# Kernel tuning notes

Hardware: AMD Instinct MI355X
Metric: run time of the kernel (lower is better)

## Reference

```python
import jax, jax.numpy as jnp
import numpy as np

B, S, HID = 2, 2048, 4096
NH, D = 32, 128          # heads, head_dim
G, GS = 8, 4             # palu groups, group_size (heads per group)
RK = 256                 # rank per K group (rank_k[i])
RV = 2048                # total V rank
FGD = RV // G            # fused_group_dim = 256
FH = FGD * NH            # fused_hidden_dim = 8192
GD = HID // G            # k group_dim = 512
THETA = 10000.0


def setup_inputs() -> dict:
    key = jax.random.key(0)
    ks = jax.random.split(key, 7)
    hidden_states = jax.random.normal(ks[0], (B, S, HID), jnp.float32)
    causal = jnp.tril(jnp.ones((S, S), bool))
    attention_mask = jnp.broadcast_to(
        jnp.where(causal, 0.0, -1e9).astype(jnp.float32)[None, None], (B, 1, S, S))
    position_ids = jnp.broadcast_to(jnp.arange(S, dtype=jnp.int32)[None], (B, S))
    sc = 0.02
    Wq = sc * jax.random.normal(ks[1], (HID, HID), jnp.float32)
    WVT = sc * jax.random.normal(ks[2], (G * RK, HID), jnp.float32)   # k_proj.VT
    U = sc * jax.random.normal(ks[3], (GD, G * RK), jnp.float32)      # k_proj.U
    Wv = sc * jax.random.normal(ks[4], (RV, HID), jnp.float32)
    Wo = sc * jax.random.normal(ks[5], (HID, FH), jnp.float32)
    return dict(hidden_states=hidden_states, attention_mask=attention_mask,
                position_ids=position_ids, Wq=Wq, WVT=WVT, U=U, Wv=Wv, Wo=Wo)


def _rotate_half(x):
    return jnp.concatenate([-x[..., D // 2:], x[..., :D // 2]], axis=-1)


def reference(hidden_states, attention_mask, position_ids, Wq, WVT, U, Wv, Wo):
    b, q, _ = hidden_states.shape
    # projections
    qs = (hidden_states @ Wq.T).reshape(b, q, NH, D).transpose(0, 2, 1, 3)      # (b,H,q,d)
    k_lat = (hidden_states @ WVT.T).reshape(b, q, G, RK).transpose(0, 2, 1, 3)  # (b,G,q,RK)
    v_lat = (hidden_states @ Wv.T).reshape(b, q, G, FGD).transpose(0, 2, 1, 3)  # (b,G,q,FGD)
    # headwise reconstruction of K: group g latent (RK) -> group_dim (512) via U[:, g-slice]
    Ug = U.reshape(GD, G, RK)
    keys = jnp.einsum('bgsr,dgr->bgsd', k_lat, Ug)                 # (b,G,q,512)
    keys = keys.transpose(0, 2, 1, 3).reshape(b, q, NH, D).transpose(0, 2, 1, 3)  # (b,H,q,d)
    # RoPE
    inv_freq = 1.0 / (THETA ** (jnp.arange(0, D, 2, dtype=jnp.float32) / D))
    freqs = position_ids.astype(jnp.float32)[..., None] * inv_freq            # (b,q,d/2)
    emb = jnp.concatenate([freqs, freqs], axis=-1)
    cos, sin = jnp.cos(emb)[:, None], jnp.sin(emb)[:, None]                   # (b,1,q,d)
    qs = qs * cos + _rotate_half(qs) * sin
    keys = keys * cos + _rotate_half(keys) * sin
    # attention scores + mask + fp32 softmax
    attn = jnp.einsum('bhqd,bhkd->bhqk', qs, keys) / np.sqrt(D).astype(np.float32)
    attn = attn + attention_mask
    attn = jax.nn.softmax(attn.astype(jnp.float32), axis=-1).astype(qs.dtype)
    # PALU fused low-rank V path: exact torch reshape/transpose semantics
    aw = attn.reshape(b, G, q * GS, q)                                        # (b,G,gs*q,kv)
    out = jnp.einsum('bgik,bgkf->bgif', aw, v_lat)                            # (b,G,gs*q,FGD)
    out = out.transpose(0, 2, 1, 3).reshape(b, q, FH)                         # (b,q,8192)
    return out @ Wo.T
```

## Files before the change

### kernel.cpp

```cpp
#include <hip/hip_runtime.h>
#include <hip/hip_bf16.h>

typedef __hip_bfloat16 bf16;
typedef __bf16 bf16x8 __attribute__((ext_vector_type(8)));
typedef float f32x4 __attribute__((ext_vector_type(4)));

#define MFMA16(a, b, c) __builtin_amdgcn_mfma_f32_16x16x32_bf16(a, b, c, 0, 0, 0)

__device__ __forceinline__ void llds16(const bf16* g, bf16* lds) {
  __builtin_amdgcn_global_load_lds(
      (const __attribute__((address_space(1))) unsigned int*)g,
      (__attribute__((address_space(3))) unsigned int*)lds, 16, 0, 0);
}

__device__ __forceinline__ void storeC(float* p, float v) { *p = v; }
__device__ __forceinline__ void storeC(bf16* p, float v) { *p = __float2bfloat16(v); }

__global__ __launch_bounds__(256) void cvt_f2b(const float* __restrict__ in,
                                               bf16* __restrict__ out, int n4) {
  int i = blockIdx.x * 256 + threadIdx.x;
  if (i >= n4) return;
  float4 v = ((const float4*)in)[i];
  union { bf16 h[4]; short4 s; } u;
  u.h[0] = __float2bfloat16(v.x);
  u.h[1] = __float2bfloat16(v.y);
  u.h[2] = __float2bfloat16(v.z);
  u.h[3] = __float2bfloat16(v.w);
  ((short4*)out)[i] = u.s;
}

template <typename OUT_T>
__global__ __launch_bounds__(512, 2) void gemm256(
    const bf16* __restrict__ A, const bf16* __restrict__ B, OUT_T* __restrict__ C,
    int K, int lda, int ldb, int ldc) {
  extern __shared__ bf16 sm[];
  const int t = threadIdx.x, w = t >> 6, l = t & 63;
  const int lane_r = l & 15, quad = l >> 4;
  const int wm = (w >> 2) * 128, wn = (w & 3) * 64;
  const long m0 = (long)blockIdx.y * 256, n0 = (long)blockIdx.x * 256;
  const int r0 = t >> 2;
  const int c0 = (((t & 3) ^ (r0 & 3)) << 3);
  const bf16* As0 = A + (m0 + r0) * lda + c0;
  const bf16* As1 = A + (m0 + r0 + 128) * lda + c0;
  const bf16* Bs0 = B + (n0 + r0) * ldb + c0;
  const bf16* Bs1 = B + (n0 + r0 + 128) * ldb + c0;

#define STAGE(sl, kt)                                   \
  do {                                                  \
    long ko = (long)(kt) * 32;                          \
    bf16* dA = sm + (sl) * 16384;                       \
    bf16* dB = dA + 8192;                               \
    llds16(As0 + ko, dA + t * 8);                       \
    llds16(As1 + ko, dA + (t + 512) * 8);               \
    llds16(Bs0 + ko, dB + t * 8);                       \
    llds16(Bs1 + ko, dB + (t + 512) * 8);               \
  } while (0)

  f32x4 acc[8][4] = {};
  const int KT = K >> 5;
  const int sw = quad ^ (lane_r & 3);

  STAGE(0, 0);
  STAGE(1, 1);
  int sl = 0;
  for (int kt = 0; kt < KT; ++kt) {
    const int pre = KT - 1 - kt;
    if (pre >= 2) {
      int sl2 = sl + 2;
      if (sl2 >= 3) sl2 -= 3;
      STAGE(sl2, kt + 2);
      asm volatile("s_waitcnt vmcnt(8)" ::: "memory");
    } else if (pre == 1) {
      asm volatile("s_waitcnt vmcnt(4)" ::: "memory");
    } else {
      asm volatile("s_waitcnt vmcnt(0)" ::: "memory");
    }
    __builtin_amdgcn_s_barrier();
    __builtin_amdgcn_sched_barrier(0);
    const bf16* Al = sm + sl * 16384;
    const bf16* Bl = Al + 8192;
    bf16x8 af[8], bfr[4];
#pragma unroll
    for (int mt = 0; mt < 8; ++mt)
      af[mt] = *(const bf16x8*)&Al[(wm + mt * 16 + lane_r) * 32 + sw * 8];
#pragma unroll
    for (int nt = 0; nt < 4; ++nt)
      bfr[nt] = *(const bf16x8*)&Bl[(wn + nt * 16 + lane_r) * 32 + sw * 8];
    __builtin_amdgcn_s_setprio(1);
#pragma unroll
    for (int mt = 0; mt < 8; ++mt)
#pragma unroll
      for (int nt = 0; nt < 4; ++nt)
        acc[mt][nt] = MFMA16(af[mt], bfr[nt], acc[mt][nt]);
    __builtin_amdgcn_s_setprio(0);
    __builtin_amdgcn_s_barrier();
    if (++sl == 3) sl = 0;
  }
#undef STAGE

#pragma unroll
  for (int mt = 0; mt < 8; ++mt)
#pragma unroll
    for (int nt = 0; nt < 4; ++nt) {
      long row = m0 + wm + mt * 16 + quad * 4;
      long col = n0 + wn + nt * 16 + lane_r;
#pragma unroll
      for (int r = 0; r < 4; ++r) storeC(&C[(row + r) * ldc + col], acc[mt][nt][r]);
    }
}

template <typename OUT_T>
__global__ __launch_bounds__(256) void gemm_bt(
    const bf16* __restrict__ A, const bf16* __restrict__ B, OUT_T* __restrict__ C,
    int M, int N, int K, int lda, int ldb, int ldc,
    long batchA, long batchB, long batchC) {
  __shared__ alignas(16) bf16 As[128 * 32];
  __shared__ alignas(16) bf16 Bs[128 * 32];
  const int t = threadIdx.x;
  const int w = t >> 6, l = t & 63;
  const int lane_r = l & 15, quad = l >> 4;
  const int wm = (w >> 1) * 64, wn = (w & 1) * 64;
  const long m0 = (long)blockIdx.y * 128, n0 = (long)blockIdx.x * 128;
  A += (long)blockIdx.z * batchA;
  B += (long)blockIdx.z * batchB;
  C += (long)blockIdx.z * batchC;
  const int r0a = t >> 2;
  const int cba = (t & 3) * 8;
  f32x4 acc[4][4] = {};
  for (int k0 = 0; k0 < K; k0 += 32) {
    llds16(A + (m0 + r0a) * lda + k0 + cba, &As[t * 8]);
    llds16(A + (m0 + r0a + 64) * lda + k0 + cba, &As[(t + 256) * 8]);
    llds16(B + (n0 + r0a) * ldb + k0 + cba, &Bs[t * 8]);
    llds16(B + (n0 + r0a + 64) * ldb + k0 + cba, &Bs[(t + 256) * 8]);
    __syncthreads();
    bf16x8 af[4], bfr[4];
#pragma unroll
    for (int mt = 0; mt < 4; ++mt)
      af[mt] = *(const bf16x8*)&As[(wm + mt * 16 + lane_r) * 32 + quad * 8];
#pragma unroll
    for (int nt = 0; nt < 4; ++nt)
      bfr[nt] = *(const bf16x8*)&Bs[(wn + nt * 16 + lane_r) * 32 + quad * 8];
#pragma unroll
    for (int mt = 0; mt < 4; ++mt)
#pragma unroll
      for (int nt = 0; nt < 4; ++nt)
        acc[mt][nt] = MFMA16(af[mt], bfr[nt], acc[mt][nt]);
    __syncthreads();
  }
#pragma unroll
  for (int mt = 0; mt < 4; ++mt)
#pragma unroll
    for (int nt = 0; nt < 4; ++nt) {
      long row = m0 + wm + mt * 16 + quad * 4;
      long col = n0 + wn + nt * 16 + lane_r;
#pragma unroll
      for (int r = 0; r < 4; ++r) storeC(&C[(row + r) * ldc + col], acc[mt][nt][r]);
    }
}

__global__ __launch_bounds__(256) void rope_perm(const bf16* __restrict__ in, int ldin,
                                                 bf16* __restrict__ out,
                                                 const int* __restrict__ pos_ids) {
  int idx = blockIdx.x * 256 + threadIdx.x;
  int d = idx & 63;
  int h = (idx >> 6) & 31;
  int bs = idx >> 11;
  int b = bs >> 11, s = bs & 2047;
  float pos = (float)pos_ids[bs];
  float inv = exp2f(-(float)d * (13.287712379549449f / 64.0f));
  float fr = pos * inv, sn, cs;
  sincosf(fr, &sn, &cs);
  long bi = (long)bs * ldin + h * 128 + d;
  long bo = ((long)(b * 32 + h) * 2048 + s) * 128 + d;
  float x1 = __bfloat162float(in[bi]);
  float x2 = __bfloat162float(in[bi + 64]);
  out[bo] = __float2bfloat16(x1 * cs - x2 * sn);
  out[bo + 64] = __float2bfloat16(x2 * cs + x1 * sn);
}

__global__ __launch_bounds__(256) void transpose_kernel(const bf16* __restrict__ v,
                                                        int ldv,
                                                        bf16* __restrict__ vt) {
  __shared__ bf16 tile[32][33];
  int b = blockIdx.z;
  int c0 = blockIdx.x * 32;
  int r0 = blockIdx.y * 32;
  int tx = threadIdx.x & 31, ty = threadIdx.x >> 5;
#pragma unroll
  for (int p = 0; p < 4; ++p) {
    int r = ty + p * 8;
    tile[r][tx] = v[((long)b * 2048 + r0 + r) * ldv + c0 + tx];
  }
  __syncthreads();
#pragma unroll
  for (int p = 0; p < 4; ++p) {
    int cidx = ty + p * 8;
    int cg = c0 + cidx;
    int g = cg >> 8, d = cg & 255;
    int s = r0 + tx;
    vt[((long)((b * 8 + g) * 64 + (s >> 5))) * 8192 + d * 32 + (s & 31)] = tile[tx][cidx];
  }
}

__global__ __launch_bounds__(512, 2) void attn_kernel(const bf16* __restrict__ Q,
                                                      const bf16* __restrict__ Kg,
                                                      const bf16* __restrict__ Vt,
                                                      bf16* __restrict__ fused) {
  __shared__ alignas(16) bf16 smem[32768];
  const int t = threadIdx.x, w = t >> 6, l = t & 63;
  const int lane_r = l & 15, quad = l >> 4;
  const int L = blockIdx.x;
  const int half = L >> 8, pair = L & 255;
  const int hb = pair >> 2, slot = pair & 3;
  const int qt = half ? slot : (7 - slot);
  const int b = hb >> 5, h = hb & 31;
  const int g = h >> 2, j = h & 3;
  const int q0 = qt * 256;
  const int qr0 = q0 + w * 32;
  const float scale = 0.08838834764831845f;

  const bf16* qbase = Q + ((long)(b * 32 + h) * 2048 + qr0 + lane_r) * 128 + quad * 8;
  bf16x8 qf[2][4];
#pragma unroll
  for (int m = 0; m < 2; ++m)
#pragma unroll
    for (int kd = 0; kd < 4; ++kd)
      qf[m][kd] = *(const bf16x8*)(qbase + m * 2048 + kd * 32);

  f32x4 acc[2][16] = {};
  float m_i[2][4], l_i[2][4];
#pragma unroll
  for (int m = 0; m < 2; ++m)
#pragma unroll
    for (int r = 0; r < 4; ++r) { m_i[m][r] = -1e30f; l_i[m][r] = 0.f; }

  const bf16* Kbase = Kg + (long)(b * 32 + h) * 262144;
  const bf16* Vtg = Vt + (long)(b * 8 + g) * 524288;
  const int kr = t >> 4, ck = (t & 15) ^ (kr & 15);
  const bf16* ksrc = Kbase + kr * 128 + ck * 8;
  const int vrA = t >> 2, cvA = (t & 3) ^ (vrA & 3);
  const int vrB = (t + 512) >> 2, cvB = ((t + 512) & 3) ^ (vrB & 3);
  const bf16* vsrcA = Vtg + vrA * 32 + cvA * 8;
  const bf16* vsrcB = Vtg + vrB * 32 + cvB * 8;

#define STAGE_T(buf, kt)                                                    \
  do {                                                                      \
    llds16(ksrc + (long)(kt) * 4096, &smem[(buf) * 4096 + t * 8]);          \
    llds16(vsrcA + (long)(kt) * 8192, &smem[8192 + (buf) * 8192 + t * 8]);  \
    llds16(vsrcB + (long)(kt) * 8192,                                       \
           &smem[8192 + (buf) * 8192 + (t + 512) * 8]);                     \
  } while (0)

  bf16* Pw = smem + 24576 + w * 1024;
  const int pslot = quad ^ ((lane_r >> 1) & 3);
  const int vslot = quad ^ (lane_r & 3);
  int poff0[4], poff1[4];
  {
    const int hi = lane_r >> 3, lo = lane_r & 7;
#pragma unroll
    for (int r = 0; r < 4; ++r) {
      int rq = quad * 4 + r;
      int sw2 = (rq >> 1) & 3;
      poff0[r] = rq * 32 + ((hi ^ sw2) << 3) + lo;
      poff1[r] = rq * 32 + (((2 + hi) ^ sw2) << 3) + lo;
    }
  }

  const int nk = qt * 8 + 8;
  const int kwmax = qt * 8 + w;

  STAGE_T(0, 0);
  for (int kt = 0; kt < nk; ++kt) {
    if (kt + 1 < nk) {
      STAGE_T((kt + 1) & 1, kt + 1);
      asm volatile("s_waitcnt vmcnt(3)" ::: "memory");
    } else {
      asm volatile("s_waitcnt vmcnt(0)" ::: "memory");
    }
    __builtin_amdgcn_s_barrier();
    __builtin_amdgcn_sched_barrier(0);
    const bf16* Ks = &smem[(kt & 1) * 4096];
    const bf16* Vs = &smem[8192 + (kt & 1) * 8192];

    if (kt <= kwmax) {
      const int k0 = kt * 32;
      const bool diag = (kt == kwmax);
      f32x4 s[2][2] = {};
#pragma unroll
      for (int ks = 0; ks < 2; ++ks) {
        bf16x8 kf[4];
#pragma unroll
        for (int kd = 0; kd < 4; ++kd) {
          int csw = (kd * 4 + quad) ^ lane_r;
          kf[kd] = *(const bf16x8*)&Ks[(ks * 16 + lane_r) * 128 + csw * 8];
        }
#pragma unroll
        for (int kd = 0; kd < 4; ++kd) {
          s[0][ks] = MFMA16(qf[0][kd], kf[kd], s[0][ks]);
          s[1][ks] = MFMA16(qf[1][kd], kf[kd], s[1][ks]);
        }
      }
      float sc[2][2][4];
      if (diag) {
#pragma unroll
        for (int m = 0; m < 2; ++m) {
          const int qrowb = qr0 + m * 16 + quad * 4;
#pragma unroll
          for (int r = 0; r < 4; ++r) {
            sc[m][0][r] = (k0 + lane_r <= qrowb + r) ? s[m][0][r] * scale : -1e30f;
            sc[m][1][r] = (k0 + 16 + lane_r <= qrowb + r) ? s[m][1][r] * scale : -1e30f;
          }
        }
      } else {
#pragma unroll
        for (int m = 0; m < 2; ++m)
#pragma unroll
          for (int r = 0; r < 4; ++r) {
            sc[m][0][r] = s[m][0][r] * scale;
            sc[m][1][r] = s[m][1][r] * scale;
          }
      }

#pragma unroll
      for (int m = 0; m < 2; ++m) {
        float mx[4];
        bool grow = false;
#pragma unroll
        for (int r = 0; r < 4; ++r) {
          float v = fmaxf(sc[m][0][r], sc[m][1][r]);
#pragma unroll
          for (int o = 1; o < 16; o <<= 1) v = fmaxf(v, __shfl_xor(v, o));
          mx[r] = v;
          grow = grow || (v > m_i[m][r]);
        }
        if (__any((int)grow)) {
#pragma unroll
          for (int r = 0; r < 4; ++r) {
            float mnew = fmaxf(m_i[m][r], mx[r]);
            float alpha = __expf(m_i[m][r] - mnew);
            m_i[m][r] = mnew;
            l_i[m][r] *= alpha;
#pragma unroll
            for (int nt = 0; nt < 16; ++nt) acc[m][nt][r] *= alpha;
          }
        }
#pragma unroll
        for (int r = 0; r < 4; ++r) {
          float p0 = __expf(sc[m][0][r] - m_i[m][r]);
          float p1 = __expf(sc[m][1][r] - m_i[m][r]);
          float rs = p0 + p1;
#pragma unroll
          for (int o = 1; o < 16; o <<= 1) rs += __shfl_xor(rs, o);
          l_i[m][r] += rs;
          Pw[m * 512 + poff0[r]] = __float2bfloat16(p0);
          Pw[m * 512 + poff1[r]] = __float2bfloat16(p1);
        }
      }

      bf16x8 pf0 = *(const bf16x8*)&Pw[lane_r * 32 + pslot * 8];
      bf16x8 pf1 = *(const bf16x8*)&Pw[(16 + lane_r) * 32 + pslot * 8];
      __builtin_amdgcn_s_setprio(1);
#pragma unroll
      for (int nt = 0; nt < 16; ++nt) {
        bf16x8 vf = *(const bf16x8*)&Vs[(nt * 16 + lane_r) * 32 + vslot * 8];
        acc[0][nt] = MFMA16(pf0, vf, acc[0][nt]);
        acc[1][nt] = MFMA16(pf1, vf, acc[1][nt]);
      }
      __builtin_amdgcn_s_setprio(0);
    }
    __builtin_amdgcn_s_barrier();
  }
#undef STAGE_T

  __syncthreads();
  bf16* EP = smem + w * 4096;
#pragma unroll
  for (int m = 0; m < 2; ++m) {
#pragma unroll
    for (int r = 0; r < 4; ++r) {
      float inv = 1.0f / l_i[m][r];
#pragma unroll
      for (int nt = 0; nt < 16; ++nt)
        EP[(quad * 4 + r) * 256 + nt * 16 + lane_r] = __float2bfloat16(acc[m][nt][r] * inv);
    }
#pragma unroll
    for (int op = 0; op < 8; ++op) {
      int row = op * 2 + (l >> 5);
      int qrow = qr0 + m * 16 + row;
      int sOut = j * 512 + (qrow >> 2), fi = qrow & 3;
      bf16x8 vread = *(const bf16x8*)&EP[row * 256 + (l & 31) * 8];
      *(bf16x8*)(fused + ((long)(b * 2048 + sOut)) * 8192 + fi * 2048 + g * 256 +
                 (l & 31) * 8) = vread;
    }
  }
}

extern "C" void kernel_launch(void* const* d_in, const int* in_sizes, int n_in,
                              void* d_out, int out_size, void* d_ws, size_t ws_size,
                              hipStream_t stream) {
  const float* hidden = (const float*)d_in[0];
  const int* pos_ids = (const int*)d_in[2];
  const float* Wq = (const float*)d_in[3];
  const float* WVT = (const float*)d_in[4];
  const float* U = (const float*)d_in[5];
  const float* Wv = (const float*)d_in[6];
  const float* Wo = (const float*)d_in[7];
  float* out = (float*)d_out;

  bf16* ws = (bf16*)d_ws;
  bf16* WB = ws;
  bf16* UB = WB + 33554432;
  bf16* hidB = UB + 1048576;
  bf16* proj = hidB + 16777216;
  bf16* Kb = proj + 33554432;
  bf16* vtB = Kb + 16777216;
  bf16* fusedB = vtB + 8388608;
  bf16* Qh = hidB;
  bf16* Kh = proj;

  static bool attr_set = false;
  if (!attr_set) {
    hipFuncSetAttribute((const void*)gemm256<bf16>,
                        hipFuncAttributeMaxDynamicSharedMemorySize, 98304);
    hipFuncSetAttribute((const void*)gemm256<float>,
                        hipFuncAttributeMaxDynamicSharedMemorySize, 98304);
    attr_set = true;
  }

  cvt_f2b<<<16384, 256, 0, stream>>>(hidden, hidB, 4194304);
  cvt_f2b<<<16384, 256, 0, stream>>>(Wq, WB, 4194304);
  cvt_f2b<<<8192, 256, 0, stream>>>(WVT, WB + 16777216, 2097152);
  cvt_f2b<<<8192, 256, 0, stream>>>(Wv, WB + 25165824, 2097152);
  gemm256<bf16><<<dim3(32, 16), 512, 98304, stream>>>(hidB, WB, proj, 4096, 4096,
                                                      4096, 8192);
  cvt_f2b<<<1024, 256, 0, stream>>>(U, UB, 262144);
  gemm_bt<bf16><<<dim3(4, 32, 8), 256, 0, stream>>>(proj + 4096, UB, Kb, 4096, 512,
                                                    256, 8192, 2048, 4096, 256, 256,
                                                    512);
  transpose_kernel<<<dim3(64, 64, 2), 256, 0, stream>>>(proj + 6144, 8192, vtB);
  rope_perm<<<32768, 256, 0, stream>>>(proj, 8192, Qh, pos_ids);
  rope_perm<<<32768, 256, 0, stream>>>(Kb, 4096, Kh, pos_ids);
  cvt_f2b<<<32768, 256, 0, stream>>>(Wo, WB, 8388608);
  attn_kernel<<<dim3(512, 1, 1), 512, 0, stream>>>(Qh, Kh, vtB, fusedB);
  gemm256<float><<<dim3(16, 16), 512, 98304, stream>>>(fusedB, WB, out, 8192, 8192,
                                                       8192, 4096);
}
```

Before: 1.193 ms.

## Use 32x32 MFMA in GEMM, XCD-aware block remap, new LDS swizzle, lazy rescale

The 256x256 GEMM now issues 32x32x16 bf16 MFMAs instead of 16x16x32, with a reworked LDS swizzle and output mapping. Blocks are remapped so each XCD covers a contiguous tile region, which is meant to improve L2 locality. The attention kernel gets a matching V swizzle change and skips the online-softmax rescale unless the running max grows by more than 8. That threshold lets exponentials exceed 1 before rescaling, trading a small overflow and precision margin for fewer rescales. The remap assumes grid dimensions divisible by 4 and 2.

```diff
diff --git a/kernel.cpp b/kernel.cpp
--- a/kernel.cpp
+++ b/kernel.cpp
@@ -4,8 +4,10 @@
 typedef __hip_bfloat16 bf16;
 typedef __bf16 bf16x8 __attribute__((ext_vector_type(8)));
 typedef float f32x4 __attribute__((ext_vector_type(4)));
+typedef float f32x16 __attribute__((ext_vector_type(16)));
 
 #define MFMA16(a, b, c) __builtin_amdgcn_mfma_f32_16x16x32_bf16(a, b, c, 0, 0, 0)
+#define MFMA32(a, b, c) __builtin_amdgcn_mfma_f32_32x32x16_bf16(a, b, c, 0, 0, 0)
 
 __device__ __forceinline__ void llds16(const bf16* g, bf16* lds) {
   __builtin_amdgcn_global_load_lds(
@@ -35,20 +37,26 @@
     int K, int lda, int ldb, int ldc) {
   extern __shared__ bf16 sm[];
   const int t = threadIdx.x, w = t >> 6, l = t & 63;
-  const int lane_r = l & 15, quad = l >> 4;
+  const int l31 = l & 31, half = l >> 5;
   const int wm = (w >> 2) * 128, wn = (w & 3) * 64;
-  const long m0 = (long)blockIdx.y * 256, n0 = (long)blockIdx.x * 256;
+  const int gx = gridDim.x;
+  const int flat = blockIdx.y * gx + blockIdx.x;
+  const int xcd = flat & 7, loc = flat >> 3;
+  const int npx = gx >> 2, npy = gridDim.y >> 1;
+  const int by = (xcd >> 2) * npy + loc / npx;
+  const int bx = (xcd & 3) * npx + loc % npx;
+  const long m0 = (long)by * 256, n0 = (long)bx * 256;
   const int r0 = t >> 2;
-  const int c0 = (((t & 3) ^ (r0 & 3)) << 3);
+  const int c0 = (((t & 3) ^ ((r0 >> 1) & 3)) << 3);
   const bf16* As0 = A + (m0 + r0) * lda + c0;
   const bf16* As1 = A + (m0 + r0 + 128) * lda + c0;
   const bf16* Bs0 = B + (n0 + r0) * ldb + c0;
   const bf16* Bs1 = B + (n0 + r0 + 128) * ldb + c0;
 
-#define STAGE(sl, kt)                                   \
+#define STAGE(sl_, kt_)                                 \
   do {                                                  \
-    long ko = (long)(kt) * 32;                          \
-    bf16* dA = sm + (sl) * 16384;                       \
+    long ko = (long)(kt_) * 32;                         \
+    bf16* dA = sm + (sl_) * 16384;                      \
     bf16* dB = dA + 8192;                               \
     llds16(As0 + ko, dA + t * 8);                       \
     llds16(As1 + ko, dA + (t + 512) * 8);               \
@@ -56,9 +64,9 @@
     llds16(Bs1 + ko, dB + (t + 512) * 8);               \
   } while (0)
 
-  f32x4 acc[8][4] = {};
+  f32x16 acc[4][2] = {};
   const int KT = K >> 5;
-  const int sw = quad ^ (lane_r & 3);
+  const int sw = (l31 >> 1) & 3;
 
   STAGE(0, 0);
   STAGE(1, 1);
@@ -79,19 +87,27 @@
     __builtin_amdgcn_sched_barrier(0);
     const bf16* Al = sm + sl * 16384;
     const bf16* Bl = Al + 8192;
-    bf16x8 af[8], bfr[4];
-#pragma unroll
-    for (int mt = 0; mt < 8; ++mt)
-      af[mt] = *(const bf16x8*)&Al[(wm + mt * 16 + lane_r) * 32 + sw * 8];
-#pragma unroll
-    for (int nt = 0; nt < 4; ++nt)
-      bfr[nt] = *(const bf16x8*)&Bl[(wn + nt * 16 + lane_r) * 32 + sw * 8];
+    bf16x8 af[4][2], bfr[2][2];
+#pragma unroll
+    for (int mt = 0; mt < 4; ++mt)
+#pragma unroll
+      for (int ks = 0; ks < 2; ++ks)
+        af[mt][ks] =
+            *(const bf16x8*)&Al[(wm + mt * 32 + l31) * 32 + (((ks * 2 + half) ^ sw) << 3)];
+#pragma unroll
+    for (int nt = 0; nt < 2; ++nt)
+#pragma unroll
+      for (int ks = 0; ks < 2; ++ks)
+        bfr[nt][ks] =
+            *(const bf16x8*)&Bl[(wn + nt * 32 + l31) * 32 + (((ks * 2 + half) ^ sw) << 3)];
     __builtin_amdgcn_s_setprio(1);
 #pragma unroll
-    for (int mt = 0; mt < 8; ++mt)
-#pragma unroll
-      for (int nt = 0; nt < 4; ++nt)
-        acc[mt][nt] = MFMA16(af[mt], bfr[nt], acc[mt][nt]);
+    for (int mt = 0; mt < 4; ++mt)
+#pragma unroll
+      for (int nt = 0; nt < 2; ++nt)
+#pragma unroll
+        for (int ks = 0; ks < 2; ++ks)
+          acc[mt][nt] = MFMA32(af[mt][ks], bfr[nt][ks], acc[mt][nt]);
     __builtin_amdgcn_s_setprio(0);
     __builtin_amdgcn_s_barrier();
     if (++sl == 3) sl = 0;
@@ -99,14 +115,15 @@
 #undef STAGE
 
 #pragma unroll
-  for (int mt = 0; mt < 8; ++mt)
-#pragma unroll
-    for (int nt = 0; nt < 4; ++nt) {
-      long row = m0 + wm + mt * 16 + quad * 4;
-      long col = n0 + wn + nt * 16 + lane_r;
-#pragma unroll
-      for (int r = 0; r < 4; ++r) storeC(&C[(row + r) * ldc + col], acc[mt][nt][r]);
-    }
+  for (int mt = 0; mt < 4; ++mt)
+#pragma unroll
+    for (int nt = 0; nt < 2; ++nt)
+#pragma unroll
+      for (int rg = 0; rg < 16; ++rg) {
+        long row = m0 + wm + mt * 32 + (rg & 3) + 8 * (rg >> 2) + 4 * half;
+        long col = n0 + wn + nt * 32 + l31;
+        storeC(&C[row * ldc + col], acc[mt][nt][rg]);
+      }
 }
 
 template <typename OUT_T>
@@ -238,8 +255,8 @@
   const bf16* Vtg = Vt + (long)(b * 8 + g) * 524288;
   const int kr = t >> 4, ck = (t & 15) ^ (kr & 15);
   const bf16* ksrc = Kbase + kr * 128 + ck * 8;
-  const int vrA = t >> 2, cvA = (t & 3) ^ (vrA & 3);
-  const int vrB = (t + 512) >> 2, cvB = ((t + 512) & 3) ^ (vrB & 3);
+  const int vrA = t >> 2, cvA = (t & 3) ^ ((vrA >> 1) & 3);
+  const int vrB = (t + 512) >> 2, cvB = (t & 3) ^ ((vrB >> 1) & 3);
   const bf16* vsrcA = Vtg + vrA * 32 + cvA * 8;
   const bf16* vsrcB = Vtg + vrB * 32 + cvB * 8;
 
@@ -253,7 +270,7 @@
 
   bf16* Pw = smem + 24576 + w * 1024;
   const int pslot = quad ^ ((lane_r >> 1) & 3);
-  const int vslot = quad ^ (lane_r & 3);
+  const int vslot = quad ^ ((lane_r >> 1) & 3);
   int poff0[4], poff1[4];
   {
     const int hi = lane_r >> 3, lo = lane_r & 7;
@@ -331,7 +348,7 @@
 #pragma unroll
           for (int o = 1; o < 16; o <<= 1) v = fmaxf(v, __shfl_xor(v, o));
           mx[r] = v;
-          grow = grow || (v > m_i[m][r]);
+          grow = grow || (v > m_i[m][r] + 8.f);
         }
         if (__any((int)grow)) {
 #pragma unroll
```

Result: no change. 1.215 ms (+1.9%).
